# Performance work log

Measured on AMD Instinct MI355X. Metric: run time of the kernel, lower is better.

## Reference

```python
import jax, jax.numpy as jnp
import numpy as np

N, A, AD, D, H, KTOP = 5, 900, 8, 256, 8, 300


def _bbox_min_max(anchor):
    # anchor: [N,A,8] = x,y,z,logw,logl,logh,sin_yaw,cos_yaw
    xyz = anchor[..., :3]
    w, l, h = [jnp.exp(anchor[..., i]) for i in (3, 4, 5)]
    sy, cy = anchor[..., 6], anchor[..., 7]
    yaw = jnp.arctan2(sy, cy)
    ca, sa = jnp.abs(jnp.cos(yaw)), jnp.abs(jnp.sin(yaw))
    ex = 0.5 * (l * ca + w * sa)
    ey = 0.5 * (l * sa + w * ca)
    half = jnp.stack([ex, ey, 0.5 * h], axis=-1)
    return xyz - half, xyz + half


def _forward(i2j_anchor, b_anchor, b_feature, transform_matrix, anchor_embed,
             w_roi, b_roi, bn_g, bn_b, fc1_w, fc1_b, fc2_w, fc2_b,
             anc_w, anc_b, lam_w, lam_b, wq, bq, wk, bk, wv, bv, wo, bo,
             ln_g, ln_b, K):
    n, a, ad = b_anchor.shape
    d = b_feature.shape[-1]
    heads = lam_w.shape[-1]
    dh = d // heads
    # ROI scoring + topk selection of anchors to broadcast to neighbors
    roi = jax.nn.sigmoid(b_feature @ w_roi + b_roi)[..., 0]              # [N,A]
    top_scores, top_idx = jax.lax.top_k(roi, K)                          # [N,K]
    conf = top_scores > 0.5                                              # [N,K]
    nbr = jnp.take_along_axis(b_feature, top_idx[..., None], axis=1)     # [N,K,D]
    idx4 = jnp.broadcast_to(top_idx[None, :, :, None], (n, n, K, ad))
    i2j_sel = jnp.take_along_axis(i2j_anchor, idx4, axis=2)              # [N,N,K,AD]
    # remove self (eye-mask): off-diagonal j per row i, row-major order
    offdiag = np.array([[j for j in range(n) if j != i] for i in range(n)])
    rows = np.arange(n)[:, None]
    m = K * (n - 1)
    i2j_rm = i2j_sel[rows, offdiag].reshape(n, m, ad)                    # [N,M,AD]
    tm_rm = transform_matrix[rows, offdiag]                              # [N,N-1,4,4]
    key_feat = nbr[offdiag].reshape(n, m, d)                             # [N,M,D]
    conf_rm = conf[offdiag].reshape(n, m, 1)
    nf_masked = key_feat * conf_rm
    # bbox-range masked aggregation of neighbor features into ego anchors
    mn, mx = _bbox_min_max(b_anchor)                                     # [N,A,3]
    centers = i2j_rm[..., :3]                                            # [N,M,3]
    inside = jnp.all((centers[:, None, :, :] >= mn[:, :, None, :]) &
                     (centers[:, None, :, :] <= mx[:, :, None, :]), axis=-1)  # [N,A,M]
    agg = jnp.einsum('nam,nmd->nad', inside.astype(b_feature.dtype), nf_masked)
    is_greater_than_range = ~jnp.any(inside, axis=1)                     # [N,M]
    b_feature = b_feature + agg
    # transform-matrix encoding: first 3 rows of 4x4 -> BN -> MLP
    mlp_in = tm_rm[:, :, :3, :].reshape(-1, 12)
    mu = mlp_in.mean(0)
    var = mlp_in.var(0)
    xbn = (mlp_in - mu) / jnp.sqrt(var + 1e-5) * bn_g + bn_b
    t = jax.nn.relu(xbn @ fc1_w + fc1_b) @ fc2_w + fc2_b                 # [N*(N-1),D]
    trans_enc = jnp.repeat(t.reshape(n, n - 1, 1, d), K, axis=2).reshape(n, m, d)
    key_pos = i2j_rm @ anc_w + anc_b + trans_enc                         # anchorencoder + trans
    # distance-biased attention mask
    diff = b_anchor[:, :, None, :2] - i2j_rm[:, None, :, :2]
    dist = jnp.sqrt(jnp.sum(diff * diff, axis=-1) + 1e-12)               # cdist [N,A,M]
    lm = (b_feature @ lam_w + lam_b).transpose(0, 2, 1)                  # [N,H,A]
    bias = -jnp.log1p(dist)[:, None, :, :] * lm[..., None]               # [N,H,A,M]
    # multi-head attention (query=b_feature(+anchor_embed pos), key/value=neighbors)
    q = b_feature + anchor_embed
    k = key_feat + key_pos
    v = key_feat
    qh = (q @ wq + bq).reshape(n, a, heads, dh)
    kh = (k @ wk + bk).reshape(n, m, heads, dh)
    vh = (v @ wv + bv).reshape(n, m, heads, dh)
    logits = jnp.einsum('nahd,nmhd->nham', qh, kh) / np.sqrt(dh).astype(np.float32) + bias
    attn = jax.nn.softmax(logits, axis=-1)
    out = jnp.einsum('nham,nmhd->nahd', attn, vh).reshape(n, a, d) @ wo + bo
    res = b_feature + out                                                # residual (identity=query)
    mu2 = res.mean(-1, keepdims=True)
    var2 = res.var(-1, keepdims=True)
    return (res - mu2) / jnp.sqrt(var2 + 1e-5) * ln_g + ln_b


def setup_inputs() -> dict:
    key = jax.random.key(0)
    ks = jax.random.split(key, 24)
    s = 0.05
    inp = {
        'i2j_anchor': jax.random.normal(ks[0], (N, N, A, AD), jnp.float32),
        'b_anchor': jax.random.normal(ks[1], (N, A, AD), jnp.float32),
        'b_feature': jax.random.normal(ks[2], (N, A, D), jnp.float32),
        'transform_matrix': jax.random.normal(ks[3], (N, N, 4, 4), jnp.float32),
        'anchor_embed': jax.random.normal(ks[4], (N, A, D), jnp.float32),
        'w_roi': jax.random.normal(ks[5], (D, 1), jnp.float32) * s,
        'b_roi': jnp.zeros((1,), jnp.float32),
        'bn_g': jnp.ones((12,), jnp.float32),
        'bn_b': jnp.zeros((12,), jnp.float32),
        'fc1_w': jax.random.normal(ks[6], (12, D), jnp.float32) * s,
        'fc1_b': jnp.zeros((D,), jnp.float32),
        'fc2_w': jax.random.normal(ks[7], (D, D), jnp.float32) * s,
        'fc2_b': jnp.zeros((D,), jnp.float32),
        'anc_w': jax.random.normal(ks[8], (AD, D), jnp.float32) * s,
        'anc_b': jnp.zeros((D,), jnp.float32),
        'lam_w': jax.random.normal(ks[9], (D, H), jnp.float32) * s,
        'lam_b': jnp.zeros((H,), jnp.float32),
        'wq': jax.random.normal(ks[10], (D, D), jnp.float32) * s,
        'bq': jnp.zeros((D,), jnp.float32),
        'wk': jax.random.normal(ks[11], (D, D), jnp.float32) * s,
        'bk': jnp.zeros((D,), jnp.float32),
        'wv': jax.random.normal(ks[12], (D, D), jnp.float32) * s,
        'bv': jnp.zeros((D,), jnp.float32),
        'wo': jax.random.normal(ks[13], (D, D), jnp.float32) * s,
        'bo': jnp.zeros((D,), jnp.float32),
        'ln_g': jnp.ones((D,), jnp.float32),
        'ln_b': jnp.zeros((D,), jnp.float32),
        'K': KTOP,
    }
    return inp


def reference(i2j_anchor, b_anchor, b_feature, transform_matrix, anchor_embed,
              w_roi, b_roi, bn_g, bn_b, fc1_w, fc1_b, fc2_w, fc2_b,
              anc_w, anc_b, lam_w, lam_b, wq, bq, wk, bk, wv, bv, wo, bo,
              ln_g, ln_b, K):
    return _forward(i2j_anchor, b_anchor, b_feature, transform_matrix, anchor_embed,
                    w_roi, b_roi, bn_g, bn_b, fc1_w, fc1_b, fc2_w, fc2_b,
                    anc_w, anc_b, lam_w, lam_b, wq, bq, wk, bk, wv, bv, wo, bo,
                    ln_g, ln_b, K)
```

## Files before the change

### kernel.cpp

```cpp
#include <hip/hip_runtime.h>
#include <math.h>

#define N_ 5
#define A_ 900
#define AD_ 8
#define D_ 256
#define H_ 8
#define DH_ 32
#define K_ 300
#define NM1_ 4
#define M_ 1200
#define MP_ 1216
#define KC_ 64
#define HALF_ 600
#define NCHUNK2_ 10

typedef _Float16 f16x8 __attribute__((ext_vector_type(8)));
typedef _Float16 f16x4 __attribute__((ext_vector_type(4)));
typedef float f32x4 __attribute__((ext_vector_type(4)));

#define LOG2E_ 1.4426950408889634f

__global__ __launch_bounds__(256) void score_kernel(const float* __restrict__ bf,
                                                    const float* __restrict__ w,
                                                    const float* __restrict__ b,
                                                    float* __restrict__ scores) {
  int wid = threadIdx.x >> 6, lane = threadIdx.x & 63;
  int row = blockIdx.x * 4 + wid;
  if (row >= N_ * A_) return;
  const float* x = bf + (long)row * D_;
  float dot = 0.f;
#pragma unroll
  for (int t = 0; t < 4; t++) dot += x[lane + 64 * t] * w[lane + 64 * t];
#pragma unroll
  for (int o = 32; o; o >>= 1) dot += __shfl_xor(dot, o, 64);
  if (lane == 0) scores[row] = 1.0f / (1.0f + expf(-(dot + b[0])));
}

__global__ __launch_bounds__(1024) void topk_kernel(const float* __restrict__ scores,
                                                    int* __restrict__ top_idx,
                                                    float* __restrict__ conf) {
  __shared__ float sc[1024];
  __shared__ int si[1024];
  int i = blockIdx.x, t = threadIdx.x;
  sc[t] = (t < A_) ? scores[i * A_ + t] : -INFINITY;
  si[t] = t;
  __syncthreads();
  for (int k = 2; k <= 1024; k <<= 1) {
    for (int j = k >> 1; j > 0; j >>= 1) {
      int ixj = t ^ j;
      if (ixj > t) {
        bool dir = ((t & k) == 0);
        float a = sc[t], b = sc[ixj];
        bool sw = dir ? (a < b) : (a > b);
        if (sw) {
          sc[t] = b; sc[ixj] = a;
          int tmp = si[t]; si[t] = si[ixj]; si[ixj] = tmp;
        }
      }
      __syncthreads();
    }
  }
  if (t < K_) {
    top_idx[i * K_ + t] = si[t];
    conf[i * K_ + t] = sc[t] > 0.5f ? 1.0f : 0.0f;
  }
}

__global__ __launch_bounds__(256) void mlp_kernel(const float* __restrict__ tm,
                                                  const float* __restrict__ bn_g, const float* __restrict__ bn_b,
                                                  const float* __restrict__ fc1_w, const float* __restrict__ fc1_b,
                                                  const float* __restrict__ fc2_w, const float* __restrict__ fc2_b,
                                                  float* __restrict__ t_out) {
  int r = blockIdx.x;
  int t = threadIdx.x;
  __shared__ float x[20][12];
  __shared__ float y[12];
  __shared__ float hbuf[D_];
  if (t < 240) {
    int rr = t / 12, f = t % 12;
    int i = rr / NM1_, jj = rr % NM1_;
    int j = jj < i ? jj : jj + 1;
    int r4 = f / 4, c4 = f % 4;
    x[rr][f] = tm[((long)(i * N_ + j) * 4 + r4) * 4 + c4];
  }
  __syncthreads();
  if (t < 12) {
    float s = 0.f;
    for (int rr = 0; rr < 20; rr++) s += x[rr][t];
    float m = s / 20.0f;
    float v = 0.f;
    for (int rr = 0; rr < 20; rr++) { float d = x[rr][t] - m; v += d * d; }
    v /= 20.0f;
    y[t] = (x[r][t] - m) * rsqrtf(v + 1e-5f) * bn_g[t] + bn_b[t];
  }
  __syncthreads();
  float acc = fc1_b[t];
#pragma unroll
  for (int f = 0; f < 12; f++) acc += y[f] * fc1_w[f * D_ + t];
  hbuf[t] = fmaxf(acc, 0.0f);
  __syncthreads();
  float acc2 = fc2_b[t];
  for (int k = 0; k < D_; k++) acc2 += hbuf[k] * fc2_w[k * D_ + t];
  t_out[r * D_ + t] = acc2;
}

#define GKT_ 10
__global__ __launch_bounds__(256) void gather_kernel(const float* __restrict__ b_feature,
                                                     const float* __restrict__ i2j_anchor,
                                                     const int* __restrict__ top_idx,
                                                     const float* __restrict__ conf,
                                                     const float* __restrict__ anc_w,
                                                     const float* __restrict__ anc_b,
                                                     const float* __restrict__ t_mlp,
                                                     _Float16* __restrict__ key_feat16,
                                                     float* __restrict__ conf_rm,
                                                     float* __restrict__ i2j_rm,
                                                     _Float16* __restrict__ key_in16) {
  int blk = blockIdx.x;
  int i = blk / NM1_, jj = blk % NM1_;
  int j = jj < i ? jj : jj + 1;
  int k0 = blockIdx.y * GKT_;
  int c = threadIdx.x;
  __shared__ float aw[AD_][D_];
#pragma unroll
  for (int r = 0; r < AD_; r++) aw[r][c] = anc_w[r * D_ + c];
  float ab = anc_b[c];
  float tv = t_mlp[(i * NM1_ + jj) * D_ + c];
  __syncthreads();
  for (int k = k0; k < k0 + GKT_; k++) {
    int idx = top_idx[j * K_ + k];
    float cf = conf[j * K_ + k];
    const float* src = b_feature + ((long)(j * A_ + idx)) * D_;
    float val = src[c];
    long mrow = (long)i * M_ + jj * K_ + k;
    key_feat16[mrow * D_ + c] = (_Float16)val;
    const float* ap = i2j_anchor + ((long)((i * N_ + j) * A_ + idx)) * AD_;
    if (c < AD_) i2j_rm[mrow * AD_ + c] = ap[c];
    if (c == 0) conf_rm[mrow] = cf;
    float pos = ab + tv;
#pragma unroll
    for (int r = 0; r < AD_; r++) pos += ap[r] * aw[r][c];
    key_in16[mrow * D_ + c] = (_Float16)(val + pos);
  }
}

__global__ __launch_bounds__(256) void trans_kernel(const float* __restrict__ w0, const float* __restrict__ w1,
                                                    const float* __restrict__ w2, const float* __restrict__ w3,
                                                    const _Float16* __restrict__ kf,
                                                    _Float16* __restrict__ wT, _Float16* __restrict__ kT) {
  int bid = blockIdx.x;
  int t = threadIdx.x;
  if (bid < 64) {
    int y = bid >> 4, tile = bid & 15;
    const float* src = (y == 0) ? w0 : (y == 1) ? w1 : (y == 2) ? w2 : w3;
    _Float16* dst = wT + (size_t)y * D_ * D_;
    int kr = (tile >> 2) * 64, nc = (tile & 3) * 64;
    __shared__ float lds[64][65];
#pragma unroll
    for (int r = 0; r < 16; r++) {
      int row = r * 4 + (t >> 6), col = t & 63;
      lds[row][col] = src[(size_t)(kr + row) * D_ + nc + col];
    }
    __syncthreads();
#pragma unroll
    for (int r = 0; r < 16; r++) {
      int orow = r * 4 + (t >> 6), ocol = t & 63;
      dst[(size_t)(nc + orow) * D_ + kr + ocol] = (_Float16)lds[ocol][orow];
    }
  } else {
    int b = bid - 64;
    int i = b / 76, rem = b % 76;
    int m0 = (rem % 19) * 64, d0 = (rem / 19) * 64;
    __shared__ _Float16 lds2[64][66];
    const _Float16* src = kf + (size_t)i * M_ * D_;
    _Float16* dst = kT + (size_t)i * D_ * M_;
#pragma unroll
    for (int r = 0; r < 16; r++) {
      int row = r * 4 + (t >> 6), col = t & 63;
      int m = m0 + row;
      lds2[row][col] = (m < M_) ? src[(size_t)m * D_ + d0 + col] : (_Float16)0.0f;
    }
    __syncthreads();
#pragma unroll
    for (int r = 0; r < 16; r++) {
      int orow = r * 4 + (t >> 6), ocol = t & 63;
      int m = m0 + ocol;
      if (m < M_) dst[(size_t)(d0 + orow) * M_ + m] = lds2[ocol][orow];
    }
  }
}

__global__ __launch_bounds__(256) void insbias_kernel(const float* __restrict__ i2j_rm,
                                                      const float* __restrict__ conf_rm,
                                                      const float* __restrict__ ban,
                                                      _Float16* __restrict__ inside,
                                                      _Float16* __restrict__ Lbuf) {
  int i = blockIdx.x;
  int g = blockIdx.y;
  __shared__ float cx[M_], cy[M_], cz[M_], cf[M_];
  for (int m = threadIdx.x; m < M_; m += 256) {
    const float* cp = i2j_rm + ((long)i * M_ + m) * AD_;
    cx[m] = cp[0]; cy[m] = cp[1]; cz[m] = cp[2];
    cf[m] = conf_rm[(long)i * M_ + m];
  }
  __syncthreads();
#pragma unroll
  for (int r = 0; r < 4; r++) {
    int a = g * 4 + r;
    int row = i * A_ + a;
    const float* ap = ban + (long)row * AD_;
    float ax = ap[0], ay = ap[1], az = ap[2];
    float w = expf(ap[3]), l = expf(ap[4]), hh = expf(ap[5]);
    float yaw = atan2f(ap[6], ap[7]);
    float ca = fabsf(cosf(yaw)), sa = fabsf(sinf(yaw));
    float ex = 0.5f * (l * ca + w * sa);
    float ey = 0.5f * (l * sa + w * ca);
    float ez = 0.5f * hh;
    float mn0 = ax - ex, mn1 = ay - ey, mn2 = az - ez;
    float mx0 = ax + ex, mx1 = ay + ey, mx2 = az + ez;
    _Float16* ldst = Lbuf + (size_t)row * MP_;
    _Float16* idst = inside + (size_t)row * M_;
    for (int m = threadIdx.x; m < M_; m += 256) {
      float c0 = cx[m], c1 = cy[m], c2 = cz[m];
      bool ins = (c0 >= mn0) && (c0 <= mx0) && (c1 >= mn1) && (c1 <= mx1) && (c2 >= mn2) && (c2 <= mx2);
      idst[m] = ins ? (_Float16)cf[m] : (_Float16)0.0f;
      float dx = ax - c0, dy = ay - c1;
      ldst[m] = (_Float16)log1pf(sqrtf(dx * dx + dy * dy + 1e-12f));
    }
  }
}

#define GLD_ 74
template <typename TO, bool HAS_BIAS, bool HAS_RES, bool VTRANS = false>
__device__ __forceinline__ void gemm_tile_body(
    const _Float16* __restrict__ A, int lda, int Mr,
    const _Float16* __restrict__ B, int ldb,
    const float* __restrict__ bias, const float* __restrict__ res,
    TO* __restrict__ C, int ldc,
    int m0, int n0, int k_begin, int k_end) {
  __shared__ _Float16 As[64 * GLD_];
  __shared__ _Float16 Bs[64 * GLD_];
  int tid = threadIdx.x;
  int lane = tid & 63;
  int wid = tid >> 6;
  int wr = (wid >> 1) * 32, wc = (wid & 1) * 32;
  int lr = lane & 15, lk = (lane >> 4) * 8;
  int srow = tid >> 3;
  int scol = (tid & 7) * 8;
  f16x8 aR[2], bR[2];
  f16x8 zero8 = {};
  auto loadg = [&](int kb) {
#pragma unroll
    for (int r = 0; r < 2; r++) {
      int gm = m0 + srow + r * 32;
      int gk = kb + scol;
      aR[r] = (gm < Mr && gk < k_end) ? *(const f16x8*)&A[(size_t)gm * lda + gk] : zero8;
      int gn = n0 + srow + r * 32;
      bR[r] = (gk < k_end) ? *(const f16x8*)&B[(size_t)gn * ldb + gk] : zero8;
    }
  };
  auto store_lds = [&]() {
#pragma unroll
    for (int r = 0; r < 2; r++) {
      *(f16x8*)&As[(srow + r * 32) * GLD_ + scol] = aR[r];
      *(f16x8*)&Bs[(srow + r * 32) * GLD_ + scol] = bR[r];
    }
  };
  f32x4 acc[2][2] = {};
  int niter = (k_end - k_begin + 63) >> 6;
  loadg(k_begin);
  store_lds();
  __syncthreads();
  for (int it = 0; it < niter; ++it) {
    bool more = (it + 1 < niter);
    if (more) loadg(k_begin + (it + 1) * 64);
#pragma unroll
    for (int ks = 0; ks < 2; ks++) {
      f16x8 af[2], bf[2];
#pragma unroll
      for (int mi = 0; mi < 2; mi++) af[mi] = *(const f16x8*)&As[(wr + mi * 16 + lr) * GLD_ + ks * 32 + lk];
#pragma unroll
      for (int ni = 0; ni < 2; ni++) bf[ni] = *(const f16x8*)&Bs[(wc + ni * 16 + lr) * GLD_ + ks * 32 + lk];
#pragma unroll
      for (int mi = 0; mi < 2; mi++)
#pragma unroll
        for (int ni = 0; ni < 2; ni++)
          acc[mi][ni] = __builtin_amdgcn_mfma_f32_16x16x32_f16(af[mi], bf[ni], acc[mi][ni], 0, 0, 0);
    }
    __syncthreads();
    if (more) { store_lds(); __syncthreads(); }
  }
  if (VTRANS) {
#pragma unroll
    for (int mi = 0; mi < 2; mi++)
#pragma unroll
      for (int ni = 0; ni < 2; ni++)
#pragma unroll
        for (int rr = 0; rr < 4; rr++) {
          int ml = wr + mi * 16 + (lane >> 4) * 4 + rr;
          int dl = wc + ni * 16 + lr;
          float v = acc[mi][ni][rr];
          if (HAS_BIAS) v += bias[n0 + dl];
          As[dl * 72 + ml] = (_Float16)v;
        }
    __syncthreads();
    int dl = tid >> 2, mp = (tid & 3) * 16;
    int gd = n0 + dl;
#pragma unroll
    for (int e8 = 0; e8 < 2; e8++) {
      int gm = m0 + mp + e8 * 8;
      if (gm < Mr) {
        int ii = gm / M_, mm = gm - ii * M_;
        *(f16x8*)&((_Float16*)C)[(size_t)(ii * D_ + gd) * ldc + mm] =
            *(const f16x8*)&As[dl * 72 + mp + e8 * 8];
      }
    }
    return;
  }
#pragma unroll
  for (int mi = 0; mi < 2; mi++)
#pragma unroll
    for (int ni = 0; ni < 2; ni++)
#pragma unroll
      for (int rr = 0; rr < 4; rr++) {
        int row = m0 + wr + mi * 16 + (lane >> 4) * 4 + rr;
        int col = n0 + wc + ni * 16 + lr;
        if (row < Mr) {
          float v = acc[mi][ni][rr];
          if (HAS_BIAS) v += bias[col];
          if (HAS_RES) v += res[(size_t)row * ldc + col];
          C[(size_t)row * ldc + col] = (TO)v;
        }
      }
}

__global__ __launch_bounds__(256) void agg_kernel(const _Float16* __restrict__ inside16,
                                                  const _Float16* __restrict__ kT16,
                                                  float* __restrict__ partial) {
  int i = blockIdx.z >> 2, sk = blockIdx.z & 3;
  int kb = sk * 320;
  int ke = kb + 320 < M_ ? kb + 320 : M_;
  gemm_tile_body<float, false, false>(
      inside16 + (size_t)i * A_ * M_, M_, A_,
      kT16 + (size_t)i * D_ * M_, M_,
      nullptr, nullptr,
      partial + (size_t)(sk * N_ + i) * A_ * D_, D_,
      blockIdx.x * 64, blockIdx.y * 64, kb, ke);
}

__global__ __launch_bounds__(256) void agg_reduce(const float* __restrict__ partial,
                                                  const float* __restrict__ b_feature,
                                                  const float* __restrict__ anchor_embed,
                                                  const float* __restrict__ lam_w,
                                                  const float* __restrict__ lam_b,
                                                  float* __restrict__ bf_upd,
                                                  _Float16* __restrict__ qin16,
                                                  float* __restrict__ lm_rm) {
  int wid = threadIdx.x >> 6, lane = threadIdx.x & 63;
  int rg = blockIdx.x * 4 + wid;
  int d0 = lane * 4;
  float lw[4][8];
#pragma unroll
  for (int e = 0; e < 4; e++) {
#pragma unroll
    for (int h = 0; h < 8; h++) lw[e][h] = lam_w[(d0 + e) * 8 + h];
  }
  float4 s = *(const float4*)&partial[(size_t)rg * D_ + d0];
#pragma unroll
  for (int sk = 1; sk < 4; sk++) {
    float4 p = *(const float4*)&partial[((size_t)sk * N_ * A_ + rg) * D_ + d0];
    s.x += p.x; s.y += p.y; s.z += p.z; s.w += p.w;
  }
  float4 bf = *(const float4*)&b_feature[(size_t)rg * D_ + d0];
  s.x += bf.x; s.y += bf.y; s.z += bf.z; s.w += bf.w;
  *(float4*)&bf_upd[(size_t)rg * D_ + d0] = s;
  float4 ae = *(const float4*)&anchor_embed[(size_t)rg * D_ + d0];
  f16x4 q4;
  q4[0] = (_Float16)(s.x + ae.x); q4[1] = (_Float16)(s.y + ae.y);
  q4[2] = (_Float16)(s.z + ae.z); q4[3] = (_Float16)(s.w + ae.w);
  *(f16x4*)&qin16[(size_t)rg * D_ + d0] = q4;
  float sv[4] = {s.x, s.y, s.z, s.w};
  float acc[8] = {};
#pragma unroll
  for (int e = 0; e < 4; e++)
#pragma unroll
    for (int h = 0; h < 8; h++) acc[h] += sv[e] * lw[e][h];
#pragma unroll
  for (int h = 0; h < 8; h++) {
#pragma unroll
    for (int o = 32; o; o >>= 1) acc[h] += __shfl_xor(acc[h], o, 64);
  }
  if (lane == 0) {
#pragma unroll
    for (int h = 0; h < 8; h++) lm_rm[(size_t)rg * H_ + h] = acc[h] + lam_b[h];
  }
}

__global__ __launch_bounds__(256) void qkv_kernel(const _Float16* __restrict__ qA,
                                                  const _Float16* __restrict__ kA,
                                                  const _Float16* __restrict__ vA,
                                                  const _Float16* __restrict__ wT,
                                                  const float* __restrict__ bq,
                                                  const float* __restrict__ bk,
                                                  const float* __restrict__ bv,
                                                  _Float16* __restrict__ qC,
                                                  _Float16* __restrict__ kC,
                                                  _Float16* __restrict__ vT) {
  int bid = blockIdx.x;
  if (bid < 284) {
    int mt = bid % 71, nt = bid / 71;
    gemm_tile_body<_Float16, true, false>(qA, D_, 4500, wT, D_, bq, nullptr, qC, D_,
                                          mt * 64, nt * 64, 0, D_);
  } else if (bid < 660) {
    int t = bid - 284;
    int mt = t % 94, nt = t / 94;
    gemm_tile_body<_Float16, true, false>(kA, D_, 6000, wT + D_ * D_, D_, bk, nullptr, kC, D_,
                                          mt * 64, nt * 64, 0, D_);
  } else {
    int t = bid - 660;
    int mt = t % 94, nt = t / 94;
    gemm_tile_body<_Float16, true, false, true>(vA, D_, 6000, wT + 2 * D_ * D_, D_, bv, nullptr, vT, MP_,
                                                mt * 64, nt * 64, 0, D_);
  }
}

__global__ __launch_bounds__(256) void outp_kernel(const _Float16* __restrict__ att16,
                                                   const _Float16* __restrict__ woT,
                                                   float* __restrict__ partial2) {
  int bid = blockIdx.x;
  int sk = bid >= 284 ? 1 : 0;
  int t = bid - sk * 284;
  int mt = t % 71, nt = t / 71;
  gemm_tile_body<float, false, false>(att16, D_, 4500, woT, D_, nullptr, nullptr,
                                      partial2 + (size_t)sk * 4500 * D_, D_,
                                      mt * 64, nt * 64, sk * 128, sk * 128 + 128);
}

#define LQP_ 72
#define LKS_ 40
__global__ __launch_bounds__(256) void attn_mfma(const _Float16* __restrict__ qh16,
                                                 const _Float16* __restrict__ kh16,
                                                 const _Float16* __restrict__ vhT,
                                                 const float* __restrict__ lm_rm,
                                                 const _Float16* __restrict__ Lbuf,
                                                 float* __restrict__ part_ms,
                                                 float* __restrict__ part_o) {
  int bid = blockIdx.x;
  int wgid = (bid & 7) * 150 + (bid >> 3);
  int ih = wgid / 30;
  int rest = wgid % 30;
  int half = rest / 15, qt = rest % 15;
  int i = ih >> 3, h = ih & 7;
  int a0 = qt * 64;
  int mbase = half * HALF_;
  int mlimit = mbase + HALF_;

  __shared__ _Float16 QP[64 * LQP_];
  __shared__ _Float16 Ks[64 * LKS_];
  __shared__ _Float16 Vs[32 * LQP_];
  __shared__ _Float16 Ls[64 * LQP_];
  __shared__ float lmvs[64];

  int tid = threadIdx.x;
  int lane = tid & 63;
  int w16 = (tid >> 6) * 16;
  int lr = lane & 15;
  int lk = (lane >> 4) * 8;
  int mq = (lane >> 4) * 4;
  int srow = tid >> 2, spiece = tid & 3;
  int vrow = tid >> 3, vpc = (tid & 7) * 8;

  {
    int aq = a0 + srow;
    int a_ld = aq < A_ ? aq : A_ - 1;
    const uint4* src = (const uint4*)(qh16 + ((long)(i * A_ + a_ld) * D_ + h * DH_));
    *(uint4*)&QP[srow * LQP_ + spiece * 8] = src[spiece];
  }
  if (tid < 64) {
    int aq = a0 + tid;
    int a_ld = aq < A_ ? aq : A_ - 1;
    lmvs[tid] = lm_rm[(long)(i * A_ + a_ld) * H_ + h];
  }

  const _Float16* kb = kh16 + (long)i * M_ * D_ + h * DH_;
  const _Float16* vb = vhT + (size_t)(i * D_ + h * DH_) * MP_;
  const _Float16* lptr[2];
#pragma unroll
  for (int rr = 0; rr < 2; rr++) {
    int aq = a0 + vrow + rr * 32;
    int a_ld = aq < A_ ? aq : A_ - 1;
    lptr[rr] = Lbuf + (size_t)(i * A_ + a_ld) * MP_ + vpc;
  }

  uint4 kvR;
  f16x8 vvR, lR[2];
  auto loadr = [&](int c) {
    int m0 = mbase + c * KC_;
    int mrow = m0 + srow;
    kvR = (mrow < M_) ? ((const uint4*)(kb + (long)mrow * D_))[spiece] : make_uint4(0, 0, 0, 0);
    vvR = *(const f16x8*)&vb[(size_t)vrow * MP_ + m0 + vpc];
#pragma unroll
    for (int rr = 0; rr < 2; rr++) lR[rr] = *(const f16x8*)&lptr[rr][m0];
  };

  __syncthreads();

  int qrow = w16 + lr;
  float lmv2 = lmvs[qrow] * LOG2E_;
  f16x8 qa = *(const f16x8*)&QP[qrow * LQP_ + lk];

  float m_run = -INFINITY, s_part = 0.0f;
  f32x4 oacc[2] = {};

  loadr(0);

  const float SC2 = 0.17677669529663687f * LOG2E_;

  for (int c = 0; c < NCHUNK2_; c++) {
    int m0 = mbase + c * KC_;
    __syncthreads();
    *(uint4*)&Ks[srow * LKS_ + spiece * 8] = kvR;
    *(f16x8*)&Vs[vrow * LQP_ + vpc] = vvR;
#pragma unroll
    for (int rr = 0; rr < 2; rr++) *(f16x8*)&Ls[(vrow + rr * 32) * LQP_ + vpc] = lR[rr];
    if (c + 1 < NCHUNK2_) loadr(c + 1);
    __syncthreads();

    f32x4 sacc[4];
#pragma unroll
    for (int mb = 0; mb < 4; mb++) {
      f16x8 kf = *(const f16x8*)&Ks[(mb * 16 + lr) * LKS_ + lk];
      sacc[mb] = __builtin_amdgcn_mfma_f32_16x16x32_f16(kf, qa, (f32x4){0.f, 0.f, 0.f, 0.f}, 0, 0, 0);
    }

    float lg[4][4];
#pragma unroll
    for (int mb = 0; mb < 4; mb++) {
      f16x4 l4 = *(const f16x4*)&Ls[qrow * LQP_ + mb * 16 + mq];
#pragma unroll
      for (int rr = 0; rr < 4; rr++) {
        int mcol = m0 + mb * 16 + mq + rr;
        float v = sacc[mb][rr] * SC2 - (float)l4[rr] * lmv2;
        lg[mb][rr] = (mcol < mlimit) ? v : -INFINITY;
      }
    }
    float cm = -INFINITY;
#pragma unroll
    for (int mb = 0; mb < 4; mb++)
#pragma unroll
      for (int rr = 0; rr < 4; rr++) cm = fmaxf(cm, lg[mb][rr]);
    cm = fmaxf(cm, __shfl_xor(cm, 16, 64));
    cm = fmaxf(cm, __shfl_xor(cm, 32, 64));
    float nm = fmaxf(m_run, cm);
    float corr = exp2f(m_run - nm);
    m_run = nm;
    float ps = 0.0f;
#pragma unroll
    for (int mb = 0; mb < 4; mb++) {
      f16x4 p4;
#pragma unroll
      for (int rr = 0; rr < 4; rr++) {
        float p = exp2f(lg[mb][rr] - nm);
        ps += p;
        p4[rr] = (_Float16)p;
      }
      *(f16x4*)&QP[qrow * LQP_ + mb * 16 + mq] = p4;
    }
    s_part = s_part * corr + ps;
#pragma unroll
    for (int r = 0; r < 4; r++) {
      float cr = __shfl(corr, (lane & 48) + mq + r, 64);
      oacc[0][r] *= cr;
      oacc[1][r] *= cr;
    }

#pragma unroll
    for (int ks = 0; ks < 2; ks++) {
      f16x8 pa = *(const f16x8*)&QP[(w16 + lr) * LQP_ + ks * 32 + lk];
#pragma unroll
      for (int db = 0; db < 2; db++) {
        f16x8 vf = *(const f16x8*)&Vs[(db * 16 + lr) * LQP_ + ks * 32 + lk];
        oacc[db] = __builtin_amdgcn_mfma_f32_16x16x32_f16(pa, vf, oacc[db], 0, 0, 0);
      }
    }
  }

  float st = s_part;
  st += __shfl_xor(st, 16, 64);
  st += __shfl_xor(st, 32, 64);

  size_t base = (size_t)(half * 40 + ih) * A_;
  if (lane < 16) {
    int a = a0 + w16 + lane;
    if (a < A_) {
      part_ms[(base + a) * 2 + 0] = m_run;
      part_ms[(base + a) * 2 + 1] = st;
    }
  }
#pragma unroll
  for (int r = 0; r < 4; r++) {
    int a = a0 + w16 + mq + r;
    if (a < A_) {
      size_t rowb = base + a;
      part_o[rowb * 32 + lr] = oacc[0][r];
      part_o[rowb * 32 + 16 + lr] = oacc[1][r];
    }
  }
}

__global__ __launch_bounds__(256) void attn_merge(const float* __restrict__ part_ms,
                                                  const float* __restrict__ part_o,
                                                  _Float16* __restrict__ att16) {
  int t = threadIdx.x;
  int R = blockIdx.x * 8 + (t >> 5);
  int d = t & 31;
  int ih = R / A_, a = R % A_;
  int i = ih >> 3, h = ih & 7;
  size_t r0 = (size_t)ih * A_ + a;
  size_t r1 = (size_t)(40 + ih) * A_ + a;
  float m0 = part_ms[r0 * 2], s0 = part_ms[r0 * 2 + 1];
  float m1 = part_ms[r1 * 2], s1 = part_ms[r1 * 2 + 1];
  float M = fmaxf(m0, m1);
  float e0 = exp2f(m0 - M), e1 = exp2f(m1 - M);
  float inv = 1.0f / (s0 * e0 + s1 * e1);
  float o = part_o[r0 * 32 + d] * e0 + part_o[r1 * 32 + d] * e1;
  att16[((size_t)(i * A_ + a)) * D_ + h * DH_ + d] = (_Float16)(o * inv);
}

__global__ __launch_bounds__(256) void ln_kernel(const float* __restrict__ partial2,
                                                 const float* __restrict__ bo,
                                                 const float* __restrict__ resid,
                                                 const float* __restrict__ g,
                                                 const float* __restrict__ b,
                                                 float* __restrict__ out) {
  int row = blockIdx.x;
  int t = threadIdx.x;
  size_t idx = (size_t)row * D_ + t;
  float v = partial2[idx] + partial2[(size_t)4500 * D_ + idx] + bo[t] + resid[idx];
  float s = v, sq = v * v;
#pragma unroll
  for (int o = 32; o; o >>= 1) {
    s += __shfl_xor(s, o, 64);
    sq += __shfl_xor(sq, o, 64);
  }
  __shared__ float ss[4], ssq[4];
  int wid = t >> 6, lane = t & 63;
  if (lane == 0) { ss[wid] = s; ssq[wid] = sq; }
  __syncthreads();
  float ts = ss[0] + ss[1] + ss[2] + ss[3];
  float tq = ssq[0] + ssq[1] + ssq[2] + ssq[3];
  float mean = ts / (float)D_;
  float var = tq / (float)D_ - mean * mean;
  out[idx] = (v - mean) * rsqrtf(var + 1e-5f) * g[t] + b[t];
}

extern "C" void kernel_launch(void* const* d_in, const int* in_sizes, int n_in,
                              void* d_out, int out_size, void* d_ws, size_t ws_size,
                              hipStream_t stream) {
  const float* i2j_anchor   = (const float*)d_in[0];
  const float* b_anchor     = (const float*)d_in[1];
  const float* b_feature    = (const float*)d_in[2];
  const float* tm           = (const float*)d_in[3];
  const float* anchor_embed = (const float*)d_in[4];
  const float* w_roi  = (const float*)d_in[5];
  const float* b_roi  = (const float*)d_in[6];
  const float* bn_g   = (const float*)d_in[7];
  const float* bn_b   = (const float*)d_in[8];
  const float* fc1_w  = (const float*)d_in[9];
  const float* fc1_b  = (const float*)d_in[10];
  const float* fc2_w  = (const float*)d_in[11];
  const float* fc2_b  = (const float*)d_in[12];
  const float* anc_w  = (const float*)d_in[13];
  const float* anc_b  = (const float*)d_in[14];
  const float* lam_w  = (const float*)d_in[15];
  const float* lam_b  = (const float*)d_in[16];
  const float* wq = (const float*)d_in[17];
  const float* bq = (const float*)d_in[18];
  const float* wk = (const float*)d_in[19];
  const float* bk = (const float*)d_in[20];
  const float* wv = (const float*)d_in[21];
  const float* bv = (const float*)d_in[22];
  const float* wo = (const float*)d_in[23];
  const float* bo = (const float*)d_in[24];
  const float* ln_g = (const float*)d_in[25];
  const float* ln_b = (const float*)d_in[26];

  float* ws = (float*)d_ws;
  size_t off = 0;
  auto alloc = [&](size_t n) { float* p = ws + off; off += (n + 3) & ~(size_t)3; return p; };

  float* scores     = alloc(N_ * A_);
  int*   top_idx    = (int*)alloc(N_ * K_);
  float* conf       = alloc(N_ * K_);
  float* t_mlp      = alloc(20 * D_);
  float* conf_rm    = alloc((size_t)N_ * M_);
  float* i2j_rm     = alloc((size_t)N_ * M_ * AD_);
  _Float16* key_feat16 = (_Float16*)alloc((size_t)N_ * M_ * D_ / 2);
  _Float16* key_in16   = (_Float16*)alloc((size_t)N_ * M_ * D_ / 2);
  _Float16* kT16       = (_Float16*)alloc((size_t)N_ * D_ * M_ / 2);
  _Float16* inside16   = (_Float16*)alloc((size_t)N_ * A_ * M_ / 2);
  _Float16* wT16       = (_Float16*)alloc((size_t)4 * D_ * D_ / 2);
  _Float16* Lbuf16     = (_Float16*)alloc((size_t)N_ * A_ * MP_ / 2 + 16);
  float* partial    = alloc((size_t)4 * N_ * A_ * D_);
  float* bf_upd     = alloc((size_t)N_ * A_ * D_);
  _Float16* qin16   = (_Float16*)alloc((size_t)N_ * A_ * D_ / 2);
  _Float16* qh16    = (_Float16*)alloc((size_t)N_ * A_ * D_ / 2);
  _Float16* kh16    = (_Float16*)alloc((size_t)N_ * M_ * D_ / 2);
  _Float16* vhT16   = (_Float16*)alloc((size_t)N_ * D_ * MP_ / 2 + 16);
  float* lm_rm      = alloc((size_t)N_ * A_ * H_);
  _Float16* att16   = (_Float16*)alloc((size_t)N_ * A_ * D_ / 2);
  float* partial2   = alloc((size_t)2 * N_ * A_ * D_);
  float* part_ms    = alloc((size_t)2 * 40 * A_ * 2);
  float* part_o     = alloc((size_t)2 * 40 * A_ * 32);

  score_kernel<<<(N_ * A_ + 3) / 4, 256, 0, stream>>>(b_feature, w_roi, b_roi, scores);
  topk_kernel<<<N_, 1024, 0, stream>>>(scores, top_idx, conf);
  mlp_kernel<<<20, 256, 0, stream>>>(tm, bn_g, bn_b, fc1_w, fc1_b, fc2_w, fc2_b, t_mlp);
  gather_kernel<<<dim3(N_ * NM1_, K_ / GKT_), 256, 0, stream>>>(b_feature, i2j_anchor, top_idx, conf,
                                                                anc_w, anc_b, t_mlp,
                                                                key_feat16, conf_rm, i2j_rm, key_in16);
  trans_kernel<<<64 + 380, 256, 0, stream>>>(wq, wk, wv, wo, key_feat16, wT16, kT16);
  insbias_kernel<<<dim3(N_, A_ / 4), 256, 0, stream>>>(i2j_rm, conf_rm, b_anchor, inside16, Lbuf16);
  agg_kernel<<<dim3(15, 4, N_ * 4), 256, 0, stream>>>(inside16, kT16, partial);
  agg_reduce<<<(N_ * A_) / 4, 256, 0, stream>>>(partial, b_feature, anchor_embed, lam_w, lam_b,
                                                bf_upd, qin16, lm_rm);
  qkv_kernel<<<284 + 376 + 376, 256, 0, stream>>>(qin16, key_in16, key_feat16, wT16,
                                                  bq, bk, bv, qh16, kh16, vhT16);
  attn_mfma<<<1200, 256, 0, stream>>>(qh16, kh16, vhT16, lm_rm, Lbuf16, part_ms, part_o);
  attn_merge<<<(40 * A_) / 8, 256, 0, stream>>>(part_ms, part_o, att16);
  outp_kernel<<<568, 256, 0, stream>>>(att16, wT16 + 3 * D_ * D_, partial2);
  ln_kernel<<<N_ * A_, 256, 0, stream>>>(partial2, bo, bf_upd, ln_g, ln_b, (float*)d_out);
}
```

Measured before the change: 176.3 us.

## Skip sigmoid in scoring, lazy softmax rescale, peel masked final attention chunk

Scores are stored as raw logits and the confidence test compares against zero, which drops the sigmoid while keeping the top-k order and the threshold. The attention loop is split so only the last chunk applies the column-limit mask. Online-softmax rescaling is skipped when no row's max grows by more than a threshold, which avoids the exp and multiplies on the accumulators. When a rescale does happen, the correction factors pass through shared memory instead of shuffles. This lazy rescale lets the fp16 probabilities exceed 1 (up to about 2^11.5), which risks precision or overflow, and it reuses the lmvs shared buffer.

```diff
diff --git a/kernel.cpp b/kernel.cpp
--- a/kernel.cpp
+++ b/kernel.cpp
@@ -34,7 +34,7 @@
   for (int t = 0; t < 4; t++) dot += x[lane + 64 * t] * w[lane + 64 * t];
 #pragma unroll
   for (int o = 32; o; o >>= 1) dot += __shfl_xor(dot, o, 64);
-  if (lane == 0) scores[row] = 1.0f / (1.0f + expf(-(dot + b[0])));
+  if (lane == 0) scores[row] = dot + b[0];
 }
 
 __global__ __launch_bounds__(1024) void topk_kernel(const float* __restrict__ scores,
@@ -63,7 +63,7 @@
   }
   if (t < K_) {
     top_idx[i * K_ + t] = si[t];
-    conf[i * K_ + t] = sc[t] > 0.5f ? 1.0f : 0.0f;
+    conf[i * K_ + t] = sc[t] > 0.0f ? 1.0f : 0.0f;
   }
 }
 
@@ -81,8 +81,7 @@
     int rr = t / 12, f = t % 12;
     int i = rr / NM1_, jj = rr % NM1_;
     int j = jj < i ? jj : jj + 1;
-    int r4 = f / 4, c4 = f % 4;
-    x[rr][f] = tm[((long)(i * N_ + j) * 4 + r4) * 4 + c4];
+    x[rr][f] = tm[((long)(i * N_ + j) * 4 + (f / 4)) * 4 + (f % 4)];
   }
   __syncthreads();
   if (t < 12) {
@@ -439,6 +438,7 @@
 
 #define LQP_ 72
 #define LKS_ 40
+#define THR2_ 11.5f
 __global__ __launch_bounds__(256) void attn_mfma(const _Float16* __restrict__ qh16,
                                                  const _Float16* __restrict__ kh16,
                                                  const _Float16* __restrict__ vhT,
@@ -517,7 +517,7 @@
 
   const float SC2 = 0.17677669529663687f * LOG2E_;
 
-  for (int c = 0; c < NCHUNK2_; c++) {
+  auto chunk_body = [&](int c, bool masked) {
     int m0 = mbase + c * KC_;
     __syncthreads();
     *(uint4*)&Ks[srow * LKS_ + spiece * 8] = kvR;
@@ -540,9 +540,12 @@
       f16x4 l4 = *(const f16x4*)&Ls[qrow * LQP_ + mb * 16 + mq];
 #pragma unroll
       for (int rr = 0; rr < 4; rr++) {
-        int mcol = m0 + mb * 16 + mq + rr;
         float v = sacc[mb][rr] * SC2 - (float)l4[rr] * lmv2;
-        lg[mb][rr] = (mcol < mlimit) ? v : -INFINITY;
+        if (masked) {
+          int mcol = m0 + mb * 16 + mq + rr;
+          v = (mcol < mlimit) ? v : -INFINITY;
+        }
+        lg[mb][rr] = v;
       }
     }
     float cm = -INFINITY;
@@ -552,27 +555,34 @@
       for (int rr = 0; rr < 4; rr++) cm = fmaxf(cm, lg[mb][rr]);
     cm = fmaxf(cm, __shfl_xor(cm, 16, 64));
     cm = fmaxf(cm, __shfl_xor(cm, 32, 64));
-    float nm = fmaxf(m_run, cm);
-    float corr = exp2f(m_run - nm);
-    m_run = nm;
+
+    bool upd = !__all(cm - m_run <= THR2_);
+    float corr = 1.0f;
+    if (upd) {
+      float nm = fmaxf(m_run, cm);
+      corr = exp2f(m_run - nm);
+      m_run = nm;
+      lmvs[qrow] = corr;
+    }
     float ps = 0.0f;
 #pragma unroll
     for (int mb = 0; mb < 4; mb++) {
       f16x4 p4;
 #pragma unroll
       for (int rr = 0; rr < 4; rr++) {
-        float p = exp2f(lg[mb][rr] - nm);
+        float p = exp2f(lg[mb][rr] - m_run);
         ps += p;
         p4[rr] = (_Float16)p;
       }
       *(f16x4*)&QP[qrow * LQP_ + mb * 16 + mq] = p4;
     }
-    s_part = s_part * corr + ps;
-#pragma unroll
-    for (int r = 0; r < 4; r++) {
-      float cr = __shfl(corr, (lane & 48) + mq + r, 64);
-      oacc[0][r] *= cr;
-      oacc[1][r] *= cr;
+    if (upd) {
+      float4 c4 = *(const float4*)&lmvs[w16 + mq];
+      s_part = s_part * corr + ps;
+      oacc[0][0] *= c4.x; oacc[0][1] *= c4.y; oacc[0][2] *= c4.z; oacc[0][3] *= c4.w;
+      oacc[1][0] *= c4.x; oacc[1][1] *= c4.y; oacc[1][2] *= c4.z; oacc[1][3] *= c4.w;
+    } else {
+      s_part += ps;
     }
 
 #pragma unroll
@@ -584,7 +594,10 @@
         oacc[db] = __builtin_amdgcn_mfma_f32_16x16x32_f16(pa, vf, oacc[db], 0, 0, 0);
       }
     }
-  }
+  };
+
+  for (int c = 0; c < NCHUNK2_ - 1; c++) chunk_body(c, false);
+  chunk_body(NCHUNK2_ - 1, true);
 
   float st = s_part;
   st += __shfl_xor(st, 16, 64);
```

Measured after the change: 172.5 us. 1.02x faster.
